# Performance work log

Measured on AMD Instinct MI355X. Metric: run time of the kernel, lower is better.

The kernel has to match this reference:

```python
import jax, jax.numpy as jnp
import numpy as np

D_MODEL = 512
N_HEADS = 8
HEAD_DIM = D_MODEL // N_HEADS
B, T = 128, 256


def setup_inputs() -> dict:
    key = jax.random.key(0)
    ks = jax.random.split(key, 5)
    s = 1.0 / np.sqrt(D_MODEL)
    return {
        "x": jax.random.normal(ks[0], (B, T, D_MODEL), dtype=jnp.float32),
        "W_qkv": jax.random.uniform(ks[1], (D_MODEL, 3 * D_MODEL), jnp.float32, -s, s),
        "b_qkv": jax.random.uniform(ks[2], (3 * D_MODEL,), jnp.float32, -s, s),
        "W_out": jax.random.uniform(ks[3], (D_MODEL, D_MODEL), jnp.float32, -s, s),
        "b_out": jax.random.uniform(ks[4], (D_MODEL,), jnp.float32, -s, s),
    }


def reference(x, W_qkv, b_qkv, W_out, b_out):
    Bsz, Tlen, C = x.shape
    H, hd = N_HEADS, HEAD_DIM
    qkv = x @ W_qkv + b_qkv                       # [B,T,3C]
    qkv = qkv.reshape(Bsz, Tlen, 3, H, hd).transpose(2, 0, 3, 1, 4)  # [3,B,H,T,hd]
    q, k, v = qkv[0], qkv[1], qkv[2]
    att = jnp.einsum('bhtd,bhsd->bhts', q, k) * (1.0 / np.sqrt(hd))  # [B,H,T,T]
    causal = jnp.tril(jnp.ones((Tlen, Tlen), dtype=bool))
    att = jnp.where(causal, att, -jnp.inf)
    att = jax.nn.softmax(att, axis=-1)
    y = jnp.einsum('bhts,bhsd->bhtd', att, v)     # [B,H,T,hd]
    y = y.transpose(0, 2, 1, 3).reshape(Bsz, Tlen, C)
    return y @ W_out + b_out
```

## Files before the change

### kernel.cpp

```cpp
#include <hip/hip_runtime.h>
#include <hip/hip_bf16.h>

typedef __attribute__((ext_vector_type(4))) float f32x4;
typedef __attribute__((ext_vector_type(8))) short s16x8;
typedef unsigned short u16;

__device__ __forceinline__ u16 f2bf(float f) {
    union { float f; unsigned int u; } a; a.f = f;
    unsigned int u = a.u;
    unsigned int lsb = (u >> 16) & 1u;
    u += 0x7fffu + lsb;
    return (u16)(u >> 16);
}

__device__ __forceinline__ void gll16(const u16* g, u16* l) {
    __builtin_amdgcn_global_load_lds(
        (const __attribute__((address_space(1))) unsigned int*)g,
        (__attribute__((address_space(3))) unsigned int*)l, 16, 0, 0);
}


__global__ void cvt_x_kernel(const float* __restrict__ x, u16* __restrict__ xb, int n4) {
    int i = blockIdx.x * 256 + threadIdx.x;
    if (i < n4) {
        float4 v = ((const float4*)x)[i];
        ushort4 o;
        o.x = f2bf(v.x); o.y = f2bf(v.y); o.z = f2bf(v.z); o.w = f2bf(v.w);
        ((ushort4*)xb)[i] = o;
    }
}

template<int KK, int NN>
__global__ void cvt_wT_kernel(const float* __restrict__ w, u16* __restrict__ wt) {
    int id = blockIdx.x * 256 + threadIdx.x;
    if (id < NN * (KK / 8)) {
        int n = id % NN, kg = id / NN;
        union { u16 h[8]; int4 v; } o;
#pragma unroll
        for (int e = 0; e < 8; ++e) o.h[e] = f2bf(w[(kg * 8 + e) * NN + n]);
        *(int4*)&wt[n * KK + kg * 8] = o.v;
    }
}


__global__ __launch_bounds__(256) void vtrans_kernel(u16* __restrict__ V) {
    __shared__ __align__(16) u16 Vl[256 * 68];
    const int tid = threadIdx.x;
    u16* base = V + ((size_t)blockIdx.x << 14);
#pragma unroll
    for (int k = 0; k < 8; ++k) {
        int g = tid + k * 256;
        int t = g >> 3, dp = g & 7;
        *(int4*)&Vl[t * 68 + dp * 8] = *(const int4*)&base[g * 8];
    }
    __syncthreads();
#pragma unroll
    for (int k = 0; k < 8; ++k) {
        int g = tid + k * 256;
        int tc = g >> 8, rem = g & 255, d = rem >> 2, p8 = rem & 3;
        int tb = tc * 32 + p8 * 8;
        union { u16 h[8]; int4 v; } o;
#pragma unroll
        for (int e = 0; e < 8; ++e) o.h[e] = Vl[(tb + e) * 68 + d];
        *(int4*)&base[g * 8] = o.v;
    }
}


template<int K>
__device__ __forceinline__ void stage256(const u16* __restrict__ A, const u16* __restrict__ Bt,
                                         int m0, int n0, int kt, u16* As, u16* Bs) {
    const int lane = threadIdx.x & 63, w = threadIdx.x >> 6;
    const int lr = lane >> 3;
    const int lg = lane & 7;
    const int sgA = lg ^ lr;
#pragma unroll
    for (int j = 0; j < 4; ++j) {
        const int blk = w * 4 + j;
        gll16(&A[(m0 + blk * 8 + lr) * K + kt + sgA * 8], &As[blk * 512]);
    }
#pragma unroll
    for (int j = 0; j < 4; ++j) {
        const int blk = w * 4 + j;
        const int sgB = lg ^ ((2 * j + (lr >> 2)) & 7);
        gll16(&Bt[(n0 + blk * 8 + lr) * K + kt + sgB * 8], &Bs[blk * 512]);
    }
}

template<int K>
__device__ __forceinline__ void gemm_tile256(const u16* __restrict__ A, const u16* __restrict__ Bt,
                                             int m0, int n0,
                                             u16* As0, u16* Bs0, u16* As1, u16* Bs1,
                                             f32x4 (&acc)[8][4]) {
    const int lane = threadIdx.x & 63, li = lane & 15, quad = lane >> 4;
    const int w = threadIdx.x >> 6;
    const int wr = w >> 2, wc = w & 3;
    const int sw = li & 7;

    stage256<K>(A, Bt, m0, n0, 0, As0, Bs0);
    __syncthreads();

#pragma unroll
    for (int kt = 0; kt < K / 64; ++kt) {
        u16* Asc = (kt & 1) ? As1 : As0;
        u16* Bsc = (kt & 1) ? Bs1 : Bs0;
        if (kt + 1 < K / 64)
            stage256<K>(A, Bt, m0, n0, (kt + 1) * 64,
                        (kt & 1) ? As0 : As1, (kt & 1) ? Bs0 : Bs1);
#pragma unroll
        for (int kc = 0; kc < 2; ++kc) {
            s16x8 af[8], bf[4];
#pragma unroll
            for (int i = 0; i < 8; ++i)
                af[i] = *(const s16x8*)&Asc[(wr * 128 + i * 16 + li) * 64 + (((quad + kc * 4) ^ sw)) * 8];
#pragma unroll
            for (int j = 0; j < 4; ++j)
                bf[j] = *(const s16x8*)&Bsc[(wc * 64 + li * 4 + j) * 64 + (((quad + kc * 4) ^ sw)) * 8];
#pragma unroll
            for (int i = 0; i < 8; ++i)
#pragma unroll
                for (int j = 0; j < 4; ++j)
                    acc[i][j] = __builtin_amdgcn_mfma_f32_16x16x32_bf16(af[i], bf[j], acc[i][j], 0, 0, 0);
        }
        __syncthreads();
    }
}


__global__ __launch_bounds__(512, 2) void gemm_qkv_kernel(const u16* __restrict__ xb,
                                                          const u16* __restrict__ WqkvT,
                                                          const float* __restrict__ b_qkv,
                                                          u16* __restrict__ Qb, u16* __restrict__ Kb,
                                                          u16* __restrict__ Vtb) {
    __shared__ __align__(16) u16 As0[256 * 64];
    __shared__ __align__(16) u16 Bs0[256 * 64];
    __shared__ __align__(16) u16 As1[256 * 64];
    __shared__ __align__(16) u16 Bs1[256 * 64];
    f32x4 acc[8][4];
#pragma unroll
    for (int i = 0; i < 8; ++i)
#pragma unroll
        for (int j = 0; j < 4; ++j) acc[i][j] = {0.f, 0.f, 0.f, 0.f};

    const int id = blockIdx.x, xcd = id & 7, slot = id >> 3;
    const int mt = xcd * 16 + slot / 6, nt = slot % 6;
    const int m0 = mt * 256, n0 = nt * 256;
    gemm_tile256<512>(xb, WqkvT, m0, n0, As0, Bs0, As1, Bs1, acc);

    const int lane = threadIdx.x & 63, li = lane & 15, quad = lane >> 4;
    const int w = threadIdx.x >> 6, wr = w >> 2, wc = w & 3;
    const int c0 = n0 + wc * 64;
    const int which = c0 >> 9, hh = (c0 >> 6) & 7;
    float4 b4 = *(const float4*)&b_qkv[c0 + li * 4];

#pragma unroll
    for (int i = 0; i < 8; ++i)
#pragma unroll
        for (int r = 0; r < 4; ++r) {
            int row = m0 + wr * 128 + i * 16 + quad * 4 + r;
            int bb = row >> 8, tt = row & 255;
            int bh = (bb * 8 + hh) << 14;
            u16 v0 = f2bf(acc[i][0][r] + b4.x), v1 = f2bf(acc[i][1][r] + b4.y);
            u16 v2 = f2bf(acc[i][2][r] + b4.z), v3 = f2bf(acc[i][3][r] + b4.w);
            if (which == 0) {
                *(ushort4*)&Qb[bh + tt * 64 + li * 4] = (ushort4){v0, v1, v2, v3};
            } else if (which == 1) {
                *(ushort4*)&Kb[bh + tt * 64 + li * 4] = (ushort4){v0, v1, v2, v3};
            } else {
                *(ushort4*)&Vtb[bh + tt * 64 + li * 4] = (ushort4){v0, v1, v2, v3};
            }
        }
}


__global__ __launch_bounds__(512, 2) void gemm_out_kernel(const u16* __restrict__ Yb,
                                                          const u16* __restrict__ WoutT,
                                                          const float* __restrict__ b_out,
                                                          float* __restrict__ out) {
    __shared__ __align__(16) u16 As0[256 * 64];
    __shared__ __align__(16) u16 Bs0[256 * 64];
    __shared__ __align__(16) u16 As1[256 * 64];
    __shared__ __align__(16) u16 Bs1[256 * 64];
    f32x4 acc[8][4];
#pragma unroll
    for (int i = 0; i < 8; ++i)
#pragma unroll
        for (int j = 0; j < 4; ++j) acc[i][j] = {0.f, 0.f, 0.f, 0.f};

    const int id = blockIdx.x, xcd = id & 7, slot = id >> 3;
    const int mt = xcd * 16 + (slot >> 1), nt = slot & 1;
    const int m0 = mt * 256, n0 = nt * 256;
    gemm_tile256<512>(Yb, WoutT, m0, n0, As0, Bs0, As1, Bs1, acc);

    const int lane = threadIdx.x & 63, li = lane & 15, quad = lane >> 4;
    const int w = threadIdx.x >> 6, wr = w >> 2, wc = w & 3;
    const int c0 = n0 + wc * 64;
    float4 b4 = *(const float4*)&b_out[c0 + li * 4];

#pragma unroll
    for (int i = 0; i < 8; ++i)
#pragma unroll
        for (int r = 0; r < 4; ++r) {
            int row = m0 + wr * 128 + i * 16 + quad * 4 + r;
            float4 o;
            o.x = acc[i][0][r] + b4.x; o.y = acc[i][1][r] + b4.y;
            o.z = acc[i][2][r] + b4.z; o.w = acc[i][3][r] + b4.w;
            *(float4*)&out[row * 512 + c0 + li * 4] = o;
        }
}


__global__ __launch_bounds__(256, 2) void attn_kernel(const u16* __restrict__ Qb,
                                                      const u16* __restrict__ Kb,
                                                      const u16* __restrict__ Vtb,
                                                      u16* __restrict__ Yb) {
    __shared__ __align__(16) u16 Ks[256 * 64];
    __shared__ __align__(16) u16 pl[4 * 2 * 16 * 40];

    const int tid = threadIdx.x, wave = tid >> 6, lane = tid & 63, li = lane & 15, quad = lane >> 4;
    const int bhid = blockIdx.x;
    const int b = bhid >> 3, h = bhid & 7;
    const int bh = bhid << 14;

    s16x8 qf0 = *(const s16x8*)&Qb[bh + (wave * 16 + li) * 64 + quad * 8];
    s16x8 qf1 = *(const s16x8*)&Qb[bh + (wave * 16 + li) * 64 + 32 + quad * 8];

    {
        const int lr = lane >> 3;
        const int sg = (lane & 7) ^ lr;
#pragma unroll
        for (int j = 0; j < 8; ++j) {
            int blk = wave * 8 + j;
            gll16(&Kb[bh + (blk * 8 + lr) * 64 + sg * 8], &Ks[blk * 512]);
        }
    }
    __syncthreads();

    u16* plw = &pl[wave * 1280];

    for (int p = 0; p < 4; ++p) {
        const int qt = p * 4 + wave;
        const int qrb = qt * 16;
        const int nst = qt + 1;

        f32x4 sacc[16];
#pragma unroll
        for (int st = 0; st < 16; ++st) sacc[st] = {0.f, 0.f, 0.f, 0.f};
        const int sw = li & 7;
#pragma unroll
        for (int g = 0; g < 4; ++g) {
            if (g * 4 < nst) {
                s16x8 kf[4][2];
#pragma unroll
                for (int t = 0; t < 4; ++t) {
                    if (g * 4 + t < nst) {
                        int rb = ((g * 4 + t) * 16 + li) * 64;
                        kf[t][0] = *(const s16x8*)&Ks[rb + ((quad    ) ^ sw) * 8];
                        kf[t][1] = *(const s16x8*)&Ks[rb + ((quad + 4) ^ sw) * 8];
                    }
                }
#pragma unroll
                for (int t = 0; t < 4; ++t) {
                    if (g * 4 + t < nst) {
                        sacc[g*4+t] = __builtin_amdgcn_mfma_f32_16x16x32_bf16(qf0, kf[t][0], sacc[g*4+t], 0, 0, 0);
                        sacc[g*4+t] = __builtin_amdgcn_mfma_f32_16x16x32_bf16(qf1, kf[t][1], sacc[g*4+t], 0, 0, 0);
                    }
                }
            }
        }

        s16x8 nqf0 = qf0, nqf1 = qf1;
        if (p < 3) {
            int nqrb = ((p + 1) * 4 + wave) * 16;
            nqf0 = *(const s16x8*)&Qb[bh + (nqrb + li) * 64 + quad * 8];
            nqf1 = *(const s16x8*)&Qb[bh + (nqrb + li) * 64 + 32 + quad * 8];
        }

        float mx[4] = {-3e38f, -3e38f, -3e38f, -3e38f};
#pragma unroll
        for (int st = 0; st < 16; ++st) {
            if (st < nst) {
                int sg2 = st * 16 + li;
#pragma unroll
                for (int r = 0; r < 4; ++r) {
                    int tg = qrb + quad * 4 + r;
                    float v = (sg2 <= tg) ? sacc[st][r] * 0.125f : -3e38f;
                    sacc[st][r] = v;
                    mx[r] = fmaxf(mx[r], v);
                }
            }
        }
#pragma unroll
        for (int d = 1; d < 16; d <<= 1)
#pragma unroll
            for (int r = 0; r < 4; ++r) mx[r] = fmaxf(mx[r], __shfl_xor(mx[r], d, 64));

        const int ns32 = (nst + 1) >> 1;
        float l[4] = {0.f, 0.f, 0.f, 0.f};
        f32x4 oacc[4];
#pragma unroll
        for (int dt = 0; dt < 4; ++dt) oacc[dt] = {0.f, 0.f, 0.f, 0.f};

        s16x8 vf[2][4];
#pragma unroll
        for (int dt = 0; dt < 4; ++dt)
            vf[0][dt] = *(const s16x8*)&Vtb[bh + (li * 4 + dt) * 32 + quad * 8];

#pragma unroll
        for (int c = 0; c < 8; ++c) {
            if (c < ns32) {
                if (c + 1 < ns32) {
#pragma unroll
                    for (int dt = 0; dt < 4; ++dt)
                        vf[(c + 1) & 1][dt] = *(const s16x8*)&Vtb[bh + (c + 1) * 2048 + (li * 4 + dt) * 32 + quad * 8];
                }
                u16* pb = plw + (c & 1) * 640;
#pragma unroll
                for (int half = 0; half < 2; ++half) {
                    int st = c * 2 + half;
#pragma unroll
                    for (int r = 0; r < 4; ++r) {
                        float e = (st < nst) ? __expf(sacc[st][r] - mx[r]) : 0.f;
                        l[r] += e;
                        pb[(quad * 4 + r) * 40 + half * 16 + li] = f2bf(e);
                    }
                }
                s16x8 pf = *(const s16x8*)&pb[li * 40 + quad * 8];
#pragma unroll
                for (int dt = 0; dt < 4; ++dt)
                    oacc[dt] = __builtin_amdgcn_mfma_f32_16x16x32_bf16(pf, vf[c & 1][dt], oacc[dt], 0, 0, 0);
            }
        }

#pragma unroll
        for (int d = 1; d < 16; d <<= 1)
#pragma unroll
            for (int r = 0; r < 4; ++r) l[r] += __shfl_xor(l[r], d, 64);

#pragma unroll
        for (int r = 0; r < 4; ++r) {
            int tg = qrb + quad * 4 + r;
            float inv = 1.0f / l[r];
            ushort4 o;
            o.x = f2bf(oacc[0][r] * inv); o.y = f2bf(oacc[1][r] * inv);
            o.z = f2bf(oacc[2][r] * inv); o.w = f2bf(oacc[3][r] * inv);
            *(ushort4*)&Yb[(b * 256 + tg) * 512 + h * 64 + li * 4] = o;
        }

        qf0 = nqf0; qf1 = nqf1;
    }
}


extern "C" void kernel_launch(void* const* d_in, const int* in_sizes, int n_in,
                              void* d_out, int out_size, void* d_ws, size_t ws_size,
                              hipStream_t stream) {
    const float* x     = (const float*)d_in[0];
    const float* W_qkv = (const float*)d_in[1];
    const float* b_qkv = (const float*)d_in[2];
    const float* W_out = (const float*)d_in[3];
    const float* b_out = (const float*)d_in[4];
    float* out = (float*)d_out;

    char* ws = (char*)d_ws;
    u16* Qb    = (u16*)(ws);
    u16* Kb    = (u16*)(ws + 33554432);
    u16* Vtb   = (u16*)(ws + 67108864);
    u16* WqkvT = (u16*)(ws + 100663296);
    u16* WoutT = (u16*)(ws + 102236160);
    u16* xb    = (u16*)(ws + 102760448);
    u16* Yb    = xb;
    if (ws_size < (size_t)136314880) return;

    cvt_x_kernel<<<16384, 256, 0, stream>>>(x, xb, 4194304);
    cvt_wT_kernel<512, 1536><<<384, 256, 0, stream>>>(W_qkv, WqkvT);
    cvt_wT_kernel<512, 512><<<128, 256, 0, stream>>>(W_out, WoutT);
    gemm_qkv_kernel<<<768, 512, 0, stream>>>(xb, WqkvT, b_qkv, Qb, Kb, Vtb);
    vtrans_kernel<<<1024, 256, 0, stream>>>(Vtb);
    attn_kernel<<<1024, 256, 0, stream>>>(Qb, Kb, Vtb, Yb);
    gemm_out_kernel<<<256, 512, 0, stream>>>(Yb, WoutT, b_out, out);
}
```

Measured before the change: 278.2 us.

## Load GEMM B operand directly from global into registers, drop B LDS staging

The shared GEMM tile routine no longer stages the weight (B) tile through LDS. Each wave loads its B fragments straight from global memory into registers, while only A keeps the double-buffered LDS path. This halves LDS usage and removes the LDS write and read traffic for B, which could allow higher occupancy. In exchange, B fragments are fetched redundantly by the two wave rows, the global loads are less coalesced, and their latency now sits on the MFMA critical path.

```diff
diff --git a/kernel.cpp b/kernel.cpp
--- a/kernel.cpp
+++ b/kernel.cpp
@@ -68,8 +68,7 @@
 
 
 template<int K>
-__device__ __forceinline__ void stage256(const u16* __restrict__ A, const u16* __restrict__ Bt,
-                                         int m0, int n0, int kt, u16* As, u16* Bs) {
+__device__ __forceinline__ void stageA256(const u16* __restrict__ A, int m0, int kt, u16* As) {
     const int lane = threadIdx.x & 63, w = threadIdx.x >> 6;
     const int lr = lane >> 3;
     const int lg = lane & 7;
@@ -79,48 +78,55 @@
         const int blk = w * 4 + j;
         gll16(&A[(m0 + blk * 8 + lr) * K + kt + sgA * 8], &As[blk * 512]);
     }
-#pragma unroll
-    for (int j = 0; j < 4; ++j) {
-        const int blk = w * 4 + j;
-        const int sgB = lg ^ ((2 * j + (lr >> 2)) & 7);
-        gll16(&Bt[(n0 + blk * 8 + lr) * K + kt + sgB * 8], &Bs[blk * 512]);
-    }
 }
 
 template<int K>
 __device__ __forceinline__ void gemm_tile256(const u16* __restrict__ A, const u16* __restrict__ Bt,
-                                             int m0, int n0,
-                                             u16* As0, u16* Bs0, u16* As1, u16* Bs1,
+                                             int m0, int n0, u16* As0, u16* As1,
                                              f32x4 (&acc)[8][4]) {
     const int lane = threadIdx.x & 63, li = lane & 15, quad = lane >> 4;
     const int w = threadIdx.x >> 6;
     const int wr = w >> 2, wc = w & 3;
     const int sw = li & 7;
-
-    stage256<K>(A, Bt, m0, n0, 0, As0, Bs0);
-    __syncthreads();
-
-#pragma unroll
-    for (int kt = 0; kt < K / 64; ++kt) {
+    constexpr int NKT = K / 64;
+    const u16* Bw = &Bt[(size_t)(n0 + wc * 64 + li * 4) * K + quad * 8];
+
+    stageA256<K>(A, m0, 0, As0);
+
+#pragma unroll
+    for (int kt = 0; kt < NKT; ++kt) {
         u16* Asc = (kt & 1) ? As1 : As0;
-        u16* Bsc = (kt & 1) ? Bs1 : Bs0;
-        if (kt + 1 < K / 64)
-            stage256<K>(A, Bt, m0, n0, (kt + 1) * 64,
-                        (kt & 1) ? As0 : As1, (kt & 1) ? Bs0 : Bs1);
-#pragma unroll
-        for (int kc = 0; kc < 2; ++kc) {
-            s16x8 af[8], bf[4];
+        s16x8 bf0[4], bf1[4];
+#pragma unroll
+        for (int j = 0; j < 4; ++j)
+            bf0[j] = *(const s16x8*)&Bw[j * K + kt * 64];
+        if (kt + 1 < NKT)
+            stageA256<K>(A, m0, (kt + 1) * 64, (kt & 1) ? As0 : As1);
+        __syncthreads();
+#pragma unroll
+        for (int j = 0; j < 4; ++j)
+            bf1[j] = *(const s16x8*)&Bw[j * K + kt * 64 + 32];
+        {
+            s16x8 af[8];
 #pragma unroll
             for (int i = 0; i < 8; ++i)
-                af[i] = *(const s16x8*)&Asc[(wr * 128 + i * 16 + li) * 64 + (((quad + kc * 4) ^ sw)) * 8];
-#pragma unroll
-            for (int j = 0; j < 4; ++j)
-                bf[j] = *(const s16x8*)&Bsc[(wc * 64 + li * 4 + j) * 64 + (((quad + kc * 4) ^ sw)) * 8];
+                af[i] = *(const s16x8*)&Asc[(wr * 128 + i * 16 + li) * 64 + ((quad ^ sw)) * 8];
 #pragma unroll
             for (int i = 0; i < 8; ++i)
 #pragma unroll
                 for (int j = 0; j < 4; ++j)
-                    acc[i][j] = __builtin_amdgcn_mfma_f32_16x16x32_bf16(af[i], bf[j], acc[i][j], 0, 0, 0);
+                    acc[i][j] = __builtin_amdgcn_mfma_f32_16x16x32_bf16(af[i], bf0[j], acc[i][j], 0, 0, 0);
+        }
+        {
+            s16x8 af[8];
+#pragma unroll
+            for (int i = 0; i < 8; ++i)
+                af[i] = *(const s16x8*)&Asc[(wr * 128 + i * 16 + li) * 64 + (((quad + 4) ^ sw)) * 8];
+#pragma unroll
+            for (int i = 0; i < 8; ++i)
+#pragma unroll
+                for (int j = 0; j < 4; ++j)
+                    acc[i][j] = __builtin_amdgcn_mfma_f32_16x16x32_bf16(af[i], bf1[j], acc[i][j], 0, 0, 0);
         }
         __syncthreads();
     }
@@ -133,9 +139,7 @@
                                                           u16* __restrict__ Qb, u16* __restrict__ Kb,
                                                           u16* __restrict__ Vtb) {
     __shared__ __align__(16) u16 As0[256 * 64];
-    __shared__ __align__(16) u16 Bs0[256 * 64];
     __shared__ __align__(16) u16 As1[256 * 64];
-    __shared__ __align__(16) u16 Bs1[256 * 64];
     f32x4 acc[8][4];
 #pragma unroll
     for (int i = 0; i < 8; ++i)
@@ -145,7 +149,7 @@
     const int id = blockIdx.x, xcd = id & 7, slot = id >> 3;
     const int mt = xcd * 16 + slot / 6, nt = slot % 6;
     const int m0 = mt * 256, n0 = nt * 256;
-    gemm_tile256<512>(xb, WqkvT, m0, n0, As0, Bs0, As1, Bs1, acc);
+    gemm_tile256<512>(xb, WqkvT, m0, n0, As0, As1, acc);
 
     const int lane = threadIdx.x & 63, li = lane & 15, quad = lane >> 4;
     const int w = threadIdx.x >> 6, wr = w >> 2, wc = w & 3;
@@ -178,9 +182,7 @@
                                                           const float* __restrict__ b_out,
                                                           float* __restrict__ out) {
     __shared__ __align__(16) u16 As0[256 * 64];
-    __shared__ __align__(16) u16 Bs0[256 * 64];
     __shared__ __align__(16) u16 As1[256 * 64];
-    __shared__ __align__(16) u16 Bs1[256 * 64];
     f32x4 acc[8][4];
 #pragma unroll
     for (int i = 0; i < 8; ++i)
@@ -190,7 +192,7 @@
     const int id = blockIdx.x, xcd = id & 7, slot = id >> 3;
     const int mt = xcd * 16 + (slot >> 1), nt = slot & 1;
     const int m0 = mt * 256, n0 = nt * 256;
-    gemm_tile256<512>(Yb, WoutT, m0, n0, As0, Bs0, As1, Bs1, acc);
+    gemm_tile256<512>(Yb, WoutT, m0, n0, As0, As1, acc);
 
     const int lane = threadIdx.x & 63, li = lane & 15, quad = lane >> 4;
     const int w = threadIdx.x >> 6, wr = w >> 2, wc = w & 3;
```

Result: slower. 315.1 us (+13.2%).
